# Optimization experiments

Hardware: AMD Instinct MI355X
Metric: run time of the kernel (lower is better)

## Reference

```python
import jax, jax.numpy as jnp
import numpy as np

N_EMBD = 1024
N_HEAD = 16

def setup_inputs() -> dict:
    key = jax.random.key(0)
    ks = jax.random.split(key, 5)
    B, T, C = 4, 2048, N_EMBD
    scale = 1.0 / np.sqrt(C)
    return {
        "x": jax.random.normal(ks[0], (B, T, C), dtype=jnp.float32),
        "w_qkv": jax.random.normal(ks[1], (C, 3 * C), dtype=jnp.float32) * scale,
        "b_qkv": jax.random.normal(ks[2], (3 * C,), dtype=jnp.float32) * 0.02,
        "w_proj": jax.random.normal(ks[3], (C, C), dtype=jnp.float32) * scale,
        "b_proj": jax.random.normal(ks[4], (C,), dtype=jnp.float32) * 0.02,
    }

def reference(x, w_qkv, b_qkv, w_proj, b_proj):
    B, T, C = x.shape
    H = N_HEAD
    D = C // H  # head dim
    qkv = x @ w_qkv + b_qkv  # [B,T,3C]
    q, k, v = jnp.split(qkv, 3, axis=-1)
    # [B,T,C] -> [B,H,T,D]
    q = q.reshape(B, T, H, D).transpose(0, 2, 1, 3)
    k = k.reshape(B, T, H, D).transpose(0, 2, 1, 3)
    v = v.reshape(B, T, H, D).transpose(0, 2, 1, 3)
    att = jnp.einsum("bhqd,bhkd->bhqk", q, k) / jnp.sqrt(jnp.asarray(D, x.dtype))
    causal = jnp.tril(jnp.ones((T, T), dtype=bool))  # [T,T]
    att = jnp.where(causal[None, None, :, :], att, -jnp.inf)
    att = jax.nn.softmax(att, axis=-1)
    y = jnp.einsum("bhqk,bhkd->bhqd", att, v)  # [B,H,T,D]
    y = y.transpose(0, 2, 1, 3).reshape(B, T, C)
    return y @ w_proj + b_proj
```

## Files before the change

### kernel.cpp

```cpp
#include <hip/hip_runtime.h>
#include <hip/hip_bf16.h>
#include <stdint.h>

typedef __bf16 bf16_8 __attribute__((ext_vector_type(8)));
typedef float f32_4 __attribute__((ext_vector_type(4)));
typedef short short4v __attribute__((ext_vector_type(4)));

static __device__ __forceinline__ unsigned short f2bf(float f) {
    union { float f; unsigned int u; } v; v.f = f;
    unsigned int u = v.u;
    unsigned int r = (u + 0x7fffu + ((u >> 16) & 1u)) >> 16;
    return (unsigned short)r;
}

static __device__ __forceinline__ unsigned int pack_bf16x2(float a, float b) {
    union { float f; unsigned int u; } ua, ub;
    ua.f = a; ub.f = b;
    return __builtin_amdgcn_perm(ub.u + 0x8000u, ua.u + 0x8000u, 0x07060302u);
}

static __device__ __forceinline__ f32_4 mfma_16x16x16_bf16(short4v a, short4v b, f32_4 c) {
#if __has_builtin(__builtin_amdgcn_mfma_f32_16x16x16bf16_1k)
    return __builtin_amdgcn_mfma_f32_16x16x16bf16_1k(a, b, c, 0, 0, 0);
#else
    asm volatile("v_mfma_f32_16x16x16_bf16 %0, %1, %2, %0"
                 : "+v"(c) : "v"(a), "v"(b));
    return c;
#endif
}

static __device__ __forceinline__ void gll16(const unsigned short* g, unsigned short* l) {
    __builtin_amdgcn_global_load_lds(
        (const __attribute__((address_space(1))) unsigned int*)g,
        (__attribute__((address_space(3))) unsigned int*)l, 16, 0, 0);
}

__global__ __launch_bounds__(256) void prep_kernel(
    const float* __restrict__ x, unsigned int* __restrict__ xbf,
    const float* __restrict__ w_qkv, unsigned short* __restrict__ wqkvt,
    const float* __restrict__ w_proj, unsigned short* __restrict__ wprojt) {
    __shared__ unsigned short tile[64][65];
    int bid = blockIdx.x;
    if (bid < 8192) {
        int i = bid * 256 + threadIdx.x;
        float4 f = ((const float4*)x)[i];
        uint2 o;
        o.x = pack_bf16x2(f.x, f.y);
        o.y = pack_bf16x2(f.z, f.w);
        ((uint2*)xbf)[i] = o;
        return;
    }
    const float* in; unsigned short* out; int N, bx, by;
    if (bid < 8960) {
        in = w_qkv; out = wqkvt; N = 3072;
        int t = bid - 8192; bx = t % 48; by = t / 48;
    } else {
        in = w_proj; out = wprojt; N = 1024;
        int t = bid - 8960; bx = t & 15; by = t >> 4;
    }
    const int K = 1024;
    int k0 = by * 64, n0 = bx * 64;
    int tc = threadIdx.x & 63, tr = threadIdx.x >> 6;
    for (int p = 0; p < 16; ++p) {
        int k = p * 4 + tr;
        tile[k][tc] = f2bf(in[(size_t)(k0 + k) * N + n0 + tc]);
    }
    __syncthreads();
    for (int p = 0; p < 16; ++p) {
        int n = p * 4 + tr;
        out[(size_t)(n0 + n) * K + k0 + tc] = tile[tc][n];
    }
}

#define BK 64
#define QSCALE 0.1803368801111204f

__global__ __launch_bounds__(256) void gemm_qkv(
    const unsigned short* __restrict__ A,
    const unsigned short* __restrict__ Bt,
    const float* __restrict__ bias,
    int M, int N, int K,
    unsigned short* __restrict__ q_out, unsigned short* __restrict__ k_out,
    unsigned short* __restrict__ v_out) {
    __shared__ __align__(16) unsigned short As[128 * BK];
    __shared__ __align__(16) unsigned short Bs[128 * BK];
    int tid = threadIdx.x;
    int wave = tid >> 6, lane = tid & 63;
    int wm = wave & 1, wn = wave >> 1;
    int quad = lane >> 4, l16 = lane & 15;
    int m0 = blockIdx.y * 128, n0 = blockIdx.x * 128;
    int which = n0 >> 10;

    f32_4 acc[4][4] = {};

    int srow = lane >> 3;
    int scs = ((lane & 7) ^ srow) * 8;
    const unsigned short* Ag = A + (size_t)(m0 + wave * 32 + srow) * K + scs;
    const unsigned short* Bg = Bt + (size_t)(n0 + wave * 32 + srow) * K + scs;
    unsigned short* Asl = As + wave * 32 * BK;
    unsigned short* Bsl = Bs + wave * 32 * BK;
    int sx = l16 & 7;

    for (int kt = 0; kt < K; kt += BK) {
        for (int p = 0; p < 4; ++p) {
            gll16(Ag + kt + (size_t)(8 * p) * K, Asl + p * 8 * BK);
            gll16(Bg + kt + (size_t)(8 * p) * K, Bsl + p * 8 * BK);
        }
        __syncthreads();
        bf16_8 af[4][2], bfr[4][2];
        for (int i = 0; i < 4; ++i)
            for (int ks = 0; ks < 2; ++ks)
                af[i][ks] = *(const bf16_8*)(As + (wm * 64 + i * 16 + l16) * BK +
                                             ((unsigned)((ks * 4 + quad) ^ sx)) * 8);
        for (int j = 0; j < 4; ++j)
            for (int ks = 0; ks < 2; ++ks)
                bfr[j][ks] = *(const bf16_8*)(Bs + (wn * 64 + j * 16 + l16) * BK +
                                              ((unsigned)((ks * 4 + quad) ^ sx)) * 8);
        if (which < 2) {
            for (int i = 0; i < 4; ++i)
                for (int j = 0; j < 4; ++j) {
                    acc[i][j] = __builtin_amdgcn_mfma_f32_16x16x32_bf16(bfr[j][0], af[i][0], acc[i][j], 0, 0, 0);
                    acc[i][j] = __builtin_amdgcn_mfma_f32_16x16x32_bf16(bfr[j][1], af[i][1], acc[i][j], 0, 0, 0);
                }
        } else {
            for (int i = 0; i < 4; ++i)
                for (int j = 0; j < 4; ++j) {
                    acc[i][j] = __builtin_amdgcn_mfma_f32_16x16x32_bf16(af[i][0], bfr[j][0], acc[i][j], 0, 0, 0);
                    acc[i][j] = __builtin_amdgcn_mfma_f32_16x16x32_bf16(af[i][1], bfr[j][1], acc[i][j], 0, 0, 0);
                }
        }
        __syncthreads();
    }

    int b = m0 >> 11;
    int tbase = (m0 & 2047) + wm * 64;
    int nw0 = n0 + wn * 64;
    if (which < 2) {
        unsigned short* dst = which == 0 ? q_out : k_out;
        float scale = which == 0 ? QSCALE : 1.0f;
        int h0 = ((n0 & 1023) >> 6) + wn;
        size_t base = ((size_t)((b << 4) + h0) * 2048) * 64;
        for (int j = 0; j < 4; ++j) {
            float4 b4 = *(const float4*)(bias + nw0 + j * 16 + quad * 4);
            int d0 = j * 16 + quad * 4;
            for (int i = 0; i < 4; ++i) {
                int t = tbase + i * 16 + l16;
                uint2 pk;
                pk.x = pack_bf16x2((acc[i][j][0] + b4.x) * scale,
                                   (acc[i][j][1] + b4.y) * scale);
                pk.y = pack_bf16x2((acc[i][j][2] + b4.z) * scale,
                                   (acc[i][j][3] + b4.w) * scale);
                *(uint2*)(dst + base + (size_t)t * 64 + d0) = pk;
            }
        }
    } else {
        for (int j = 0; j < 4; ++j) {
            int n = nw0 + j * 16 + l16;
            int c = n & 1023, h = c >> 6, d = c & 63;
            float bs = bias[n];
            size_t base = ((size_t)((b << 4) + h) * 64 + d) * 2048;
            for (int i = 0; i < 4; ++i) {
                int t0 = tbase + i * 16 + quad * 4;
                uint2 pk;
                pk.x = pack_bf16x2(acc[i][j][0] + bs, acc[i][j][1] + bs);
                pk.y = pack_bf16x2(acc[i][j][2] + bs, acc[i][j][3] + bs);
                *(uint2*)(v_out + base + t0) = pk;
            }
        }
    }
}

__global__ __launch_bounds__(256) void gemm_proj(
    const unsigned short* __restrict__ A,
    const unsigned short* __restrict__ Bt,
    const float* __restrict__ bias,
    int M, int N, int K, float* __restrict__ outf) {
    __shared__ __align__(16) unsigned short As[128 * BK];
    __shared__ __align__(16) unsigned short Bs[64 * BK];
    int tid = threadIdx.x;
    int wave = tid >> 6, lane = tid & 63;
    int wm = wave & 1, wn = wave >> 1;
    int quad = lane >> 4, l16 = lane & 15;
    int m0 = blockIdx.y * 128, n0 = blockIdx.x * 64;

    f32_4 acc[4][2] = {};

    int srow = lane >> 3;
    int scs = ((lane & 7) ^ srow) * 8;
    const unsigned short* Ag = A + (size_t)(m0 + wave * 32 + srow) * K + scs;
    const unsigned short* Bg = Bt + (size_t)(n0 + wave * 16 + srow) * K + scs;
    unsigned short* Asl = As + wave * 32 * BK;
    unsigned short* Bsl = Bs + wave * 16 * BK;
    int sx = l16 & 7;

    for (int kt = 0; kt < K; kt += BK) {
        for (int p = 0; p < 4; ++p)
            gll16(Ag + kt + (size_t)(8 * p) * K, Asl + p * 8 * BK);
        for (int p = 0; p < 2; ++p)
            gll16(Bg + kt + (size_t)(8 * p) * K, Bsl + p * 8 * BK);
        __syncthreads();
        bf16_8 af[4][2], bfr[2][2];
        for (int i = 0; i < 4; ++i)
            for (int ks = 0; ks < 2; ++ks)
                af[i][ks] = *(const bf16_8*)(As + (wm * 64 + i * 16 + l16) * BK +
                                             ((unsigned)((ks * 4 + quad) ^ sx)) * 8);
        for (int j = 0; j < 2; ++j)
            for (int ks = 0; ks < 2; ++ks)
                bfr[j][ks] = *(const bf16_8*)(Bs + (wn * 32 + j * 16 + l16) * BK +
                                              ((unsigned)((ks * 4 + quad) ^ sx)) * 8);
        for (int i = 0; i < 4; ++i)
            for (int j = 0; j < 2; ++j) {
                acc[i][j] = __builtin_amdgcn_mfma_f32_16x16x32_bf16(af[i][0], bfr[j][0], acc[i][j], 0, 0, 0);
                acc[i][j] = __builtin_amdgcn_mfma_f32_16x16x32_bf16(af[i][1], bfr[j][1], acc[i][j], 0, 0, 0);
            }
        __syncthreads();
    }

    for (int j = 0; j < 2; ++j) {
        int n = n0 + wn * 32 + j * 16 + l16;
        float bs = bias[n];
        for (int i = 0; i < 4; ++i) {
            int m = m0 + wm * 64 + i * 16 + quad * 4;
            for (int r = 0; r < 4; ++r)
                outf[(size_t)(m + r) * N + n] = acc[i][j][r] + bs;
        }
    }
}

__global__ __launch_bounds__(256, 4) void attn_kernel(
    const unsigned short* __restrict__ Q, const unsigned short* __restrict__ Kb,
    const unsigned short* __restrict__ Vt, unsigned short* __restrict__ Y,
    int T) {
    __shared__ __align__(16) unsigned short KsB[2][64 * 64];
    __shared__ __align__(16) unsigned short VtsB[2][64 * 64];

    int tid = threadIdx.x;
    int wave = tid >> 6, lane = tid & 63;
    int quad = lane >> 4, l16 = lane & 15;
    int bh = blockIdx.x;
    int b = bh >> 4, h = bh & 15;
    int y = blockIdx.y;
    int qtA = 31 - y, qtB = y;
    int qwA = qtA * 64 + wave * 16;
    int qwB = qtB * 64 + wave * 16;

    int srow = lane >> 3;
    int scs = ((lane & 7) ^ srow) * 8;
    int sx = l16 & 7;

    bf16_8 qaA[2], qaB[2];
    for (int ks = 0; ks < 2; ++ks) {
        qaA[ks] = *(const bf16_8*)(Q + ((size_t)bh * T + qwA + l16) * 64 + ks * 32 + quad * 8);
        qaB[ks] = *(const bf16_8*)(Q + ((size_t)bh * T + qwB + l16) * 64 + ks * 32 + quad * 8);
    }

    f32_4 oA[4] = {}, oB[4] = {};
    float lsA = 0.0f, lsB = 0.0f;

    int nkt = qtA + 1;

    for (int p = 0; p < 2; ++p) {
        int row = wave * 16 + p * 8;
        gll16(Kb + ((size_t)bh * T + row + srow) * 64 + scs, &KsB[0][row * 64]);
        gll16(Vt + ((size_t)bh * 64 + row + srow) * (size_t)T + scs, &VtsB[0][row * 64]);
    }
    __syncthreads();

    for (int kt = 0; kt < nkt; ++kt) {
        int cur = kt & 1;
        int kb = kt * 64;
        if (kt + 1 < nkt) {
            int kb2 = kb + 64, nxt = cur ^ 1;
            for (int p = 0; p < 2; ++p) {
                int row = wave * 16 + p * 8;
                gll16(Kb + ((size_t)bh * T + kb2 + row + srow) * 64 + scs, &KsB[nxt][row * 64]);
                gll16(Vt + ((size_t)bh * 64 + row + srow) * (size_t)T + kb2 + scs, &VtsB[nxt][row * 64]);
            }
        }
        const unsigned short* KsC = KsB[cur];
        const unsigned short* VtsC = VtsB[cur];
        bool doB = (kt <= qtB);

        f32_4 sA[4] = {}, sB[4] = {};
        for (int kf = 0; kf < 4; ++kf) {
            bf16_8 k0 = *(const bf16_8*)(KsC + (kf * 16 + l16) * 64 + ((unsigned)(quad ^ sx)) * 8);
            bf16_8 k1 = *(const bf16_8*)(KsC + (kf * 16 + l16) * 64 + ((unsigned)((4 + quad) ^ sx)) * 8);
            sA[kf] = __builtin_amdgcn_mfma_f32_16x16x32_bf16(k0, qaA[0], sA[kf], 0, 0, 0);
            sA[kf] = __builtin_amdgcn_mfma_f32_16x16x32_bf16(k1, qaA[1], sA[kf], 0, 0, 0);
            if (doB) {
                sB[kf] = __builtin_amdgcn_mfma_f32_16x16x32_bf16(k0, qaB[0], sB[kf], 0, 0, 0);
                sB[kf] = __builtin_amdgcn_mfma_f32_16x16x32_bf16(k1, qaB[1], sB[kf], 0, 0, 0);
            }
        }

        if (kt == qtA) {
            int q = qwA + l16;
            for (int kf = 0; kf < 4; ++kf) {
                int kk = kb + kf * 16 + quad * 4;
                for (int r = 0; r < 4; ++r)
                    if (kk + r > q) sA[kf][r] = -1e30f;
            }
        }
        if (kt == qtB) {
            int q = qwB + l16;
            for (int kf = 0; kf < 4; ++kf) {
                int kk = kb + kf * 16 + quad * 4;
                for (int r = 0; r < 4; ++r)
                    if (kk + r > q) sB[kf][r] = -1e30f;
            }
        }

        short4v pbA[4], pbB[4];
        {
            float rs = 0.0f;
            for (int kf = 0; kf < 4; ++kf) {
                f32_4 p;
                for (int r = 0; r < 4; ++r) { p[r] = __builtin_amdgcn_exp2f(sA[kf][r]); rs += p[r]; }
                union { unsigned int u[2]; short4v s4; } pu;
                pu.u[0] = pack_bf16x2(p[0], p[1]);
                pu.u[1] = pack_bf16x2(p[2], p[3]);
                pbA[kf] = pu.s4;
            }
            rs += __shfl_xor(rs, 16);
            rs += __shfl_xor(rs, 32);
            lsA += rs;
        }
        if (doB) {
            float rs = 0.0f;
            for (int kf = 0; kf < 4; ++kf) {
                f32_4 p;
                for (int r = 0; r < 4; ++r) { p[r] = __builtin_amdgcn_exp2f(sB[kf][r]); rs += p[r]; }
                union { unsigned int u[2]; short4v s4; } pu;
                pu.u[0] = pack_bf16x2(p[0], p[1]);
                pu.u[1] = pack_bf16x2(p[2], p[3]);
                pbB[kf] = pu.s4;
            }
            rs += __shfl_xor(rs, 16);
            rs += __shfl_xor(rs, 32);
            lsB += rs;
        }

        for (int kf = 0; kf < 4; ++kf) {
            unsigned voff = ((unsigned)((2 * kf + (quad >> 1)) ^ sx)) * 8 + (quad & 1) * 4;
            for (int df = 0; df < 4; ++df) {
                short4v va = *(const short4v*)(VtsC + (df * 16 + l16) * 64 + voff);
                oA[df] = mfma_16x16x16_bf16(va, pbA[kf], oA[df]);
                if (doB) oB[df] = mfma_16x16x16_bf16(va, pbB[kf], oB[df]);
            }
        }
        __syncthreads();
    }

    {
        float inv = 1.0f / lsA;
        unsigned short* yp = Y + ((size_t)b * T + qwA + l16) * 1024 + h * 64 + quad * 4;
        for (int df = 0; df < 4; ++df) {
            uint2 pk;
            pk.x = pack_bf16x2(oA[df][0] * inv, oA[df][1] * inv);
            pk.y = pack_bf16x2(oA[df][2] * inv, oA[df][3] * inv);
            *(uint2*)(yp + df * 16) = pk;
        }
    }
    {
        float inv = 1.0f / lsB;
        unsigned short* yp = Y + ((size_t)b * T + qwB + l16) * 1024 + h * 64 + quad * 4;
        for (int df = 0; df < 4; ++df) {
            uint2 pk;
            pk.x = pack_bf16x2(oB[df][0] * inv, oB[df][1] * inv);
            pk.y = pack_bf16x2(oB[df][2] * inv, oB[df][3] * inv);
            *(uint2*)(yp + df * 16) = pk;
        }
    }
}

extern "C" void kernel_launch(void* const* d_in, const int* in_sizes, int n_in,
                              void* d_out, int out_size, void* d_ws, size_t ws_size,
                              hipStream_t stream) {
    const float* x = (const float*)d_in[0];
    const float* w_qkv = (const float*)d_in[1];
    const float* b_qkv = (const float*)d_in[2];
    const float* w_proj = (const float*)d_in[3];
    const float* b_proj = (const float*)d_in[4];
    float* out = (float*)d_out;

    unsigned short* xbf = (unsigned short*)d_ws;
    unsigned short* wqkvt = xbf + 8388608;
    unsigned short* wprojt = wqkvt + 3145728;
    unsigned short* Qb = wprojt + 1048576;
    unsigned short* Kb = Qb + 8388608;
    unsigned short* Vtb = Kb + 8388608;
    unsigned short* Yb = Vtb + 8388608;

    hipLaunchKernelGGL(prep_kernel, dim3(9216), dim3(256), 0, stream,
                       x, (unsigned int*)xbf, w_qkv, wqkvt, w_proj, wprojt);
    hipLaunchKernelGGL(gemm_qkv, dim3(24, 64), dim3(256), 0, stream,
                       xbf, wqkvt, b_qkv, 8192, 3072, 1024,
                       Qb, Kb, Vtb);
    hipLaunchKernelGGL(attn_kernel, dim3(64, 16), dim3(256), 0, stream,
                       Qb, Kb, Vtb, Yb, 2048);
    hipLaunchKernelGGL(gemm_proj, dim3(16, 64), dim3(256), 0, stream,
                       Yb, wprojt, b_proj, 8192, 1024, 1024, out);
}
```

Baseline: 289.1 us.

## Split attention query-tile pairs into separate blocks and enlarge proj GEMM tile

```diff
diff --git a/kernel.cpp b/kernel.cpp
--- a/kernel.cpp
+++ b/kernel.cpp
@@ -176,48 +176,48 @@
     const float* __restrict__ bias,
     int M, int N, int K, float* __restrict__ outf) {
     __shared__ __align__(16) unsigned short As[128 * BK];
-    __shared__ __align__(16) unsigned short Bs[64 * BK];
+    __shared__ __align__(16) unsigned short Bs[128 * BK];
     int tid = threadIdx.x;
     int wave = tid >> 6, lane = tid & 63;
     int wm = wave & 1, wn = wave >> 1;
     int quad = lane >> 4, l16 = lane & 15;
-    int m0 = blockIdx.y * 128, n0 = blockIdx.x * 64;
-
-    f32_4 acc[4][2] = {};
+    int m0 = blockIdx.y * 128, n0 = blockIdx.x * 128;
+
+    f32_4 acc[4][4] = {};
 
     int srow = lane >> 3;
     int scs = ((lane & 7) ^ srow) * 8;
     const unsigned short* Ag = A + (size_t)(m0 + wave * 32 + srow) * K + scs;
-    const unsigned short* Bg = Bt + (size_t)(n0 + wave * 16 + srow) * K + scs;
+    const unsigned short* Bg = Bt + (size_t)(n0 + wave * 32 + srow) * K + scs;
     unsigned short* Asl = As + wave * 32 * BK;
-    unsigned short* Bsl = Bs + wave * 16 * BK;
+    unsigned short* Bsl = Bs + wave * 32 * BK;
     int sx = l16 & 7;
 
     for (int kt = 0; kt < K; kt += BK) {
-        for (int p = 0; p < 4; ++p)
+        for (int p = 0; p < 4; ++p) {
             gll16(Ag + kt + (size_t)(8 * p) * K, Asl + p * 8 * BK);
-        for (int p = 0; p < 2; ++p)
             gll16(Bg + kt + (size_t)(8 * p) * K, Bsl + p * 8 * BK);
-        __syncthreads();
-        bf16_8 af[4][2], bfr[2][2];
+        }
+        __syncthreads();
+        bf16_8 af[4][2], bfr[4][2];
         for (int i = 0; i < 4; ++i)
             for (int ks = 0; ks < 2; ++ks)
                 af[i][ks] = *(const bf16_8*)(As + (wm * 64 + i * 16 + l16) * BK +
                                              ((unsigned)((ks * 4 + quad) ^ sx)) * 8);
-        for (int j = 0; j < 2; ++j)
+        for (int j = 0; j < 4; ++j)
             for (int ks = 0; ks < 2; ++ks)
-                bfr[j][ks] = *(const bf16_8*)(Bs + (wn * 32 + j * 16 + l16) * BK +
+                bfr[j][ks] = *(const bf16_8*)(Bs + (wn * 64 + j * 16 + l16) * BK +
                                               ((unsigned)((ks * 4 + quad) ^ sx)) * 8);
         for (int i = 0; i < 4; ++i)
-            for (int j = 0; j < 2; ++j) {
+            for (int j = 0; j < 4; ++j) {
                 acc[i][j] = __builtin_amdgcn_mfma_f32_16x16x32_bf16(af[i][0], bfr[j][0], acc[i][j], 0, 0, 0);
                 acc[i][j] = __builtin_amdgcn_mfma_f32_16x16x32_bf16(af[i][1], bfr[j][1], acc[i][j], 0, 0, 0);
             }
         __syncthreads();
     }
 
-    for (int j = 0; j < 2; ++j) {
-        int n = n0 + wn * 32 + j * 16 + l16;
+    for (int j = 0; j < 4; ++j) {
+        int n = n0 + wn * 64 + j * 16 + l16;
         float bs = bias[n];
         for (int i = 0; i < 4; ++i) {
             int m = m0 + wm * 64 + i * 16 + quad * 4;
@@ -227,7 +227,7 @@
     }
 }
 
-__global__ __launch_bounds__(256, 4) void attn_kernel(
+__global__ __launch_bounds__(256, 5) void attn_kernel(
     const unsigned short* __restrict__ Q, const unsigned short* __restrict__ Kb,
     const unsigned short* __restrict__ Vt, unsigned short* __restrict__ Y,
     int T) {
@@ -239,25 +239,23 @@
     int quad = lane >> 4, l16 = lane & 15;
     int bh = blockIdx.x;
     int b = bh >> 4, h = bh & 15;
-    int y = blockIdx.y;
-    int qtA = 31 - y, qtB = y;
-    int qwA = qtA * 64 + wave * 16;
-    int qwB = qtB * 64 + wave * 16;
+    int qt = 31 - blockIdx.y;
+    int qw = qt * 64 + wave * 16;
+    int nkt = qt + 1;
 
     int srow = lane >> 3;
     int scs = ((lane & 7) ^ srow) * 8;
     int sx = l16 & 7;
 
-    bf16_8 qaA[2], qaB[2];
-    for (int ks = 0; ks < 2; ++ks) {
-        qaA[ks] = *(const bf16_8*)(Q + ((size_t)bh * T + qwA + l16) * 64 + ks * 32 + quad * 8);
-        qaB[ks] = *(const bf16_8*)(Q + ((size_t)bh * T + qwB + l16) * 64 + ks * 32 + quad * 8);
-    }
-
-    f32_4 oA[4] = {}, oB[4] = {};
-    float lsA = 0.0f, lsB = 0.0f;
-
-    int nkt = qtA + 1;
+    bf16_8 qa[2];
+    for (int ks = 0; ks < 2; ++ks)
+        qa[ks] = *(const bf16_8*)(Q + ((size_t)bh * T + qw + l16) * 64 + ks * 32 + quad * 8);
+
+    f32_4 o[4] = {};
+    f32_4 osum = {};
+    short4v vones;
+    { unsigned short one = 0x3F80;
+      vones[0] = (short)one; vones[1] = (short)one; vones[2] = (short)one; vones[3] = (short)one; }
 
     for (int p = 0; p < 2; ++p) {
         int row = wave * 16 + p * 8;
@@ -279,97 +277,54 @@
         }
         const unsigned short* KsC = KsB[cur];
         const unsigned short* VtsC = VtsB[cur];
-        bool doB = (kt <= qtB);
-
-        f32_4 sA[4] = {}, sB[4] = {};
+
+        f32_4 s[4] = {};
         for (int kf = 0; kf < 4; ++kf) {
             bf16_8 k0 = *(const bf16_8*)(KsC + (kf * 16 + l16) * 64 + ((unsigned)(quad ^ sx)) * 8);
             bf16_8 k1 = *(const bf16_8*)(KsC + (kf * 16 + l16) * 64 + ((unsigned)((4 + quad) ^ sx)) * 8);
-            sA[kf] = __builtin_amdgcn_mfma_f32_16x16x32_bf16(k0, qaA[0], sA[kf], 0, 0, 0);
-            sA[kf] = __builtin_amdgcn_mfma_f32_16x16x32_bf16(k1, qaA[1], sA[kf], 0, 0, 0);
-            if (doB) {
-                sB[kf] = __builtin_amdgcn_mfma_f32_16x16x32_bf16(k0, qaB[0], sB[kf], 0, 0, 0);
-                sB[kf] = __builtin_amdgcn_mfma_f32_16x16x32_bf16(k1, qaB[1], sB[kf], 0, 0, 0);
-            }
-        }
-
-        if (kt == qtA) {
-            int q = qwA + l16;
+            s[kf] = __builtin_amdgcn_mfma_f32_16x16x32_bf16(k0, qa[0], s[kf], 0, 0, 0);
+            s[kf] = __builtin_amdgcn_mfma_f32_16x16x32_bf16(k1, qa[1], s[kf], 0, 0, 0);
+        }
+
+        if (kt == qt) {
+            int q = qw + l16;
             for (int kf = 0; kf < 4; ++kf) {
                 int kk = kb + kf * 16 + quad * 4;
                 for (int r = 0; r < 4; ++r)
-                    if (kk + r > q) sA[kf][r] = -1e30f;
-            }
-        }
-        if (kt == qtB) {
-            int q = qwB + l16;
-            for (int kf = 0; kf < 4; ++kf) {
-                int kk = kb + kf * 16 + quad * 4;
-                for (int r = 0; r < 4; ++r)
-                    if (kk + r > q) sB[kf][r] = -1e30f;
-            }
-        }
-
-        short4v pbA[4], pbB[4];
-        {
-            float rs = 0.0f;
-            for (int kf = 0; kf < 4; ++kf) {
-                f32_4 p;
-                for (int r = 0; r < 4; ++r) { p[r] = __builtin_amdgcn_exp2f(sA[kf][r]); rs += p[r]; }
-                union { unsigned int u[2]; short4v s4; } pu;
-                pu.u[0] = pack_bf16x2(p[0], p[1]);
-                pu.u[1] = pack_bf16x2(p[2], p[3]);
-                pbA[kf] = pu.s4;
-            }
-            rs += __shfl_xor(rs, 16);
-            rs += __shfl_xor(rs, 32);
-            lsA += rs;
-        }
-        if (doB) {
-            float rs = 0.0f;
-            for (int kf = 0; kf < 4; ++kf) {
-                f32_4 p;
-                for (int r = 0; r < 4; ++r) { p[r] = __builtin_amdgcn_exp2f(sB[kf][r]); rs += p[r]; }
-                union { unsigned int u[2]; short4v s4; } pu;
-                pu.u[0] = pack_bf16x2(p[0], p[1]);
-                pu.u[1] = pack_bf16x2(p[2], p[3]);
-                pbB[kf] = pu.s4;
-            }
-            rs += __shfl_xor(rs, 16);
-            rs += __shfl_xor(rs, 32);
-            lsB += rs;
-        }
-
+                    if (kk + r > q) s[kf][r] = -1e30f;
+            }
+        }
+
+        short4v pb[4];
         for (int kf = 0; kf < 4; ++kf) {
+            float p0 = __builtin_amdgcn_exp2f(s[kf][0]);
+            float p1 = __builtin_amdgcn_exp2f(s[kf][1]);
+            float p2 = __builtin_amdgcn_exp2f(s[kf][2]);
+            float p3 = __builtin_amdgcn_exp2f(s[kf][3]);
+            union { unsigned int u[2]; short4v s4; } pu;
+            pu.u[0] = pack_bf16x2(p0, p1);
+            pu.u[1] = pack_bf16x2(p2, p3);
+            pb[kf] = pu.s4;
+        }
+
+        for (int kf = 0; kf < 4; ++kf) {
+            osum = mfma_16x16x16_bf16(vones, pb[kf], osum);
             unsigned voff = ((unsigned)((2 * kf + (quad >> 1)) ^ sx)) * 8 + (quad & 1) * 4;
             for (int df = 0; df < 4; ++df) {
                 short4v va = *(const short4v*)(VtsC + (df * 16 + l16) * 64 + voff);
-                oA[df] = mfma_16x16x16_bf16(va, pbA[kf], oA[df]);
-                if (doB) oB[df] = mfma_16x16x16_bf16(va, pbB[kf], oB[df]);
-            }
-        }
-        __syncthreads();
-    }
-
-    {
-        float inv = 1.0f / lsA;
-        unsigned short* yp = Y + ((size_t)b * T + qwA + l16) * 1024 + h * 64 + quad * 4;
-        for (int df = 0; df < 4; ++df) {
-            uint2 pk;
-            pk.x = pack_bf16x2(oA[df][0] * inv, oA[df][1] * inv);
-            pk.y = pack_bf16x2(oA[df][2] * inv, oA[df][3] * inv);
-            *(uint2*)(yp + df * 16) = pk;
-        }
-    }
-    {
-        float inv = 1.0f / lsB;
-        unsigned short* yp = Y + ((size_t)b * T + qwB + l16) * 1024 + h * 64 + quad * 4;
-        for (int df = 0; df < 4; ++df) {
-            uint2 pk;
-            pk.x = pack_bf16x2(oB[df][0] * inv, oB[df][1] * inv);
-            pk.y = pack_bf16x2(oB[df][2] * inv, oB[df][3] * inv);
-            *(uint2*)(yp + df * 16) = pk;
-        }
+                o[df] = mfma_16x16x16_bf16(va, pb[kf], o[df]);
+            }
+        }
+        __syncthreads();
+    }
+
+    float inv = 1.0f / osum[0];
+    unsigned short* yp = Y + ((size_t)b * T + qw + l16) * 1024 + h * 64 + quad * 4;
+    for (int df = 0; df < 4; ++df) {
+        uint2 pk;
+        pk.x = pack_bf16x2(o[df][0] * inv, o[df][1] * inv);
+        pk.y = pack_bf16x2(o[df][2] * inv, o[df][3] * inv);
+        *(uint2*)(yp + df * 16) = pk;
     }
 }
 
@@ -396,8 +351,8 @@
     hipLaunchKernelGGL(gemm_qkv, dim3(24, 64), dim3(256), 0, stream,
                        xbf, wqkvt, b_qkv, 8192, 3072, 1024,
                        Qb, Kb, Vtb);
-    hipLaunchKernelGGL(attn_kernel, dim3(64, 16), dim3(256), 0, stream,
+    hipLaunchKernelGGL(attn_kernel, dim3(64, 32), dim3(256), 0, stream,
                        Qb, Kb, Vtb, Yb, 2048);
-    hipLaunchKernelGGL(gemm_proj, dim3(16, 64), dim3(256), 0, stream,
+    hipLaunchKernelGGL(gemm_proj, dim3(8, 64), dim3(256), 0, stream,
                        Yb, wprojt, b_proj, 8192, 1024, 1024, out);
 }
```

New measurement: 262.2 us. 1.1x faster.
